# Kernel optimization log

Hardware: AMD Instinct MI355X
Metric: run time of the kernel (lower is better)

Reference implementation:

```python
import jax, jax.numpy as jnp
import numpy as np

DIM = 512
NUM_HEADS = 8
HEAD_DIM = DIM // NUM_HEADS
SCALE = HEAD_DIM ** -0.5


def setup_inputs() -> dict:
    key = jax.random.key(0)
    kx, kqw, kqb, kpw, kpb = jax.random.split(key, 5)
    B, N = 2, 4096
    x = jax.random.normal(kx, (B, N, DIM), dtype=jnp.float32)
    # nn.Linear weights stored as [out, in]; init ~ U(-1/sqrt(in), 1/sqrt(in))
    bound = 1.0 / np.sqrt(DIM)
    qkv_w = jax.random.uniform(kqw, (3 * DIM, DIM), minval=-bound, maxval=bound, dtype=jnp.float32)
    qkv_b = jax.random.uniform(kqb, (3 * DIM,), minval=-bound, maxval=bound, dtype=jnp.float32)
    proj_w = jax.random.uniform(kpw, (DIM, DIM), minval=-bound, maxval=bound, dtype=jnp.float32)
    proj_b = jax.random.uniform(kpb, (DIM,), minval=-bound, maxval=bound, dtype=jnp.float32)
    return {"x": x, "qkv_w": qkv_w, "qkv_b": qkv_b, "proj_w": proj_w, "proj_b": proj_b}


def reference(x, qkv_w, qkv_b, proj_w, proj_b):
    B, N, C = x.shape
    # qkv: [B, N, 3C] -> [3, B, H, N, Dh]
    qkv = x @ qkv_w.T + qkv_b
    qkv = qkv.reshape(B, N, 3, NUM_HEADS, HEAD_DIM).transpose(2, 0, 3, 1, 4)
    q, k, v = qkv[0], qkv[1], qkv[2]
    # scores: [B, H, N, N] (materialized, matching the original math)
    attn = jnp.einsum("bhqd,bhkd->bhqk", q, k) * SCALE
    attn = jax.nn.softmax(attn, axis=-1)
    out = jnp.einsum("bhqk,bhkd->bhqd", attn, v)  # [B, H, N, Dh]
    out = out.transpose(0, 2, 1, 3).reshape(B, N, C)
    return out @ proj_w.T + proj_b
```

## Files before the change

### kernel.cpp

```cpp
#include <hip/hip_runtime.h>
#include <hip/hip_bf16.h>
#include <stdint.h>
#include <stddef.h>

typedef __attribute__((ext_vector_type(8))) short short8;
typedef __attribute__((ext_vector_type(4))) float f32x4;

#define MFMA16(a, b, c) __builtin_amdgcn_mfma_f32_16x16x32_bf16((a), (b), (c), 0, 0, 0)

#define QSCALE 0.1803368801111204f

#if __has_builtin(__builtin_amdgcn_exp2f)
#define EXP2(x) __builtin_amdgcn_exp2f(x)
#else
#define EXP2(x) __builtin_exp2f(x)
#endif

__device__ __forceinline__ float b2f(short x) {
    unsigned u = ((unsigned)(unsigned short)x) << 16;
    float f; __builtin_memcpy(&f, &u, 4); return f;
}
__device__ __forceinline__ short f2b(float f) {
    unsigned u; __builtin_memcpy(&u, &f, 4);
    u = (u + 0x7FFFu + ((u >> 16) & 1u)) >> 16;
    return (short)u;
}
__device__ __forceinline__ unsigned pack2(float a, float b) {
    unsigned ua, ub; __builtin_memcpy(&ua, &a, 4); __builtin_memcpy(&ub, &b, 4);
    return __builtin_amdgcn_perm(ub + 0x8000u, ua + 0x8000u, 0x07060302u);
}
__device__ __forceinline__ short8 load8f(const float* p) {
    const float4 f0 = *(const float4*)p;
    const float4 f1 = *(const float4*)(p + 4);
    short8 r;
    r[0]=f2b(f0.x); r[1]=f2b(f0.y); r[2]=f2b(f0.z); r[3]=f2b(f0.w);
    r[4]=f2b(f1.x); r[5]=f2b(f1.y); r[6]=f2b(f1.z); r[7]=f2b(f1.w);
    return r;
}

__global__ __launch_bounds__(256) void cvt3(
    const float* __restrict__ s0, short* __restrict__ d0, int n0,
    const float* __restrict__ s1, short* __restrict__ d1, int n1,
    const float* __restrict__ s2, short* __restrict__ d2, int n2)
{
    int i = blockIdx.x * 256 + threadIdx.x;
    if (i < n0) { *(short8*)(d0 + (size_t)i * 8) = load8f(s0 + (size_t)i * 8); return; }
    i -= n0;
    if (i < n1) { *(short8*)(d1 + (size_t)i * 8) = load8f(s1 + (size_t)i * 8); return; }
    i -= n1;
    if (i < n2) { *(short8*)(d2 + (size_t)i * 8) = load8f(s2 + (size_t)i * 8); }
}

__global__ __launch_bounds__(256) void qkv_gemm(
    const short* __restrict__ X, const short* __restrict__ W,
    const float* __restrict__ bias,
    short* __restrict__ Qb, short* __restrict__ Kb, short* __restrict__ Vb)
{
    __shared__ short sT[128][132];

    const int tid  = threadIdx.x;
    const int wv   = tid >> 6;
    const int lane = tid & 63;
    const int l15  = lane & 15;
    const int quad = lane >> 4;
    const int m0   = blockIdx.x * 128 + (wv >> 1) * 64;
    const int sec  = blockIdx.y >> 2;
    const int bis  = blockIdx.y & 3;
    const int nbase = sec * 512 + bis * 128;
    const int j0   = (wv & 1) * 64;

    const f32x4 zero = {0.f, 0.f, 0.f, 0.f};
    f32x4 acc[4][4];
#pragma unroll
    for (int i = 0; i < 4; i++)
#pragma unroll
        for (int j = 0; j < 4; j++) acc[i][j] = zero;

    for (int k0 = 0; k0 < 512; k0 += 32) {
        short8 a[4], b[4];
#pragma unroll
        for (int i = 0; i < 4; i++)
            a[i] = *(const short8*)(X + (size_t)(m0 + i * 16 + l15) * 512 + k0 + quad * 8);
#pragma unroll
        for (int j = 0; j < 4; j++)
            b[j] = *(const short8*)(W + (size_t)(nbase + j0 + j * 16 + l15) * 512 + k0 + quad * 8);
#pragma unroll
        for (int i = 0; i < 4; i++)
#pragma unroll
            for (int j = 0; j < 4; j++)
                acc[i][j] = MFMA16(a[i], b[j], acc[i][j]);
    }

    if (sec < 2) {
        const float scale = (sec == 0) ? QSCALE : 1.0f;
        short* dst = (sec == 0) ? Qb : Kb;
#pragma unroll
        for (int j = 0; j < 4; j++) {
            const int jc = bis * 128 + j0 + j * 16 + l15;
            const float bs = bias[sec * 512 + jc];
            const int hl = jc >> 6, d = jc & 63;
#pragma unroll
            for (int i = 0; i < 4; i++) {
#pragma unroll
                for (int r = 0; r < 4; r++) {
                    const int m = m0 + i * 16 + quad * 4 + r;
                    const int bb = m >> 12, seq = m & 4095;
                    dst[((size_t)(bb * 8 + hl) * 4096 + seq) * 64 + d] =
                        f2b((acc[i][j][r] + bs) * scale);
                }
            }
        }
    } else {
#pragma unroll
        for (int j = 0; j < 4; j++) {
            const int jcl = j0 + j * 16 + l15;
            const float bs = bias[nbase + jcl];
#pragma unroll
            for (int i = 0; i < 4; i++) {
                uint2 w;
                w.x = pack2(acc[i][j][0] + bs, acc[i][j][1] + bs);
                w.y = pack2(acc[i][j][2] + bs, acc[i][j][3] + bs);
                *(uint2*)&sT[jcl][(wv >> 1) * 64 + i * 16 + quad * 4] = w;
            }
        }
        __syncthreads();

        const int jcl = tid >> 1, half = tid & 1;
        const int hl = (bis * 128 + jcl) >> 6;
        const int d  = jcl & 63;
        const int bb = (blockIdx.x * 128) >> 12;
        const int seq0 = ((blockIdx.x * 128) & 4095) + half * 64;
        short* dst = Vb + ((size_t)(bb * 8 + hl) * 64 + d) * 4096 + seq0;
#pragma unroll
        for (int u = 0; u < 8; u++)
            *(short8*)(dst + u * 8) = *(const short8*)&sT[jcl][half * 64 + u * 8];
    }
}

__global__ __launch_bounds__(256) void flash_attn(
    const short* __restrict__ Q, const short* __restrict__ K,
    const short* __restrict__ V, short* __restrict__ PO0,
    short* __restrict__ PO1, float* __restrict__ lbuf, int ktiles)
{
    __shared__ short sK[64][72];
    __shared__ short sV[64][72];
    __shared__ short sP[4][16][72];

    const int tid  = threadIdx.x;
    const int wv   = tid >> 6;
    const int lane = tid & 63;
    const int l15  = lane & 15;
    const int quad = lane >> 4;
    const int bh = blockIdx.y;
    const int b = bh >> 3, h = bh & 7;
    const int qw = blockIdx.x * 128 + wv * 32;
    const int ks = blockIdx.z;
    const int key0 = ks * ktiles * 64;

    const short* Qb = Q + (size_t)bh * 4096 * 64;
    const short* Kb = K + (size_t)bh * 4096 * 64;
    const short* Vb = V + (size_t)bh * 64 * 4096;

    const short8 aq00 = *(const short8*)(Qb + (size_t)(qw + l15) * 64 + quad * 8);
    const short8 aq01 = *(const short8*)(Qb + (size_t)(qw + l15) * 64 + 32 + quad * 8);
    const short8 aq10 = *(const short8*)(Qb + (size_t)(qw + 16 + l15) * 64 + quad * 8);
    const short8 aq11 = *(const short8*)(Qb + (size_t)(qw + 16 + l15) * 64 + 32 + quad * 8);

    const f32x4 zero = {0.f, 0.f, 0.f, 0.f};
    f32x4 o0[4], o1[4];
    f32x4 lac0 = zero, lac1 = zero;
#pragma unroll
    for (int r = 0; r < 4; r++) { o0[r] = zero; o1[r] = zero; }
    const short one_bf = (short)0x3F80;
    const short8 ones = {one_bf, one_bf, one_bf, one_bf,
                         one_bf, one_bf, one_bf, one_bf};

    int srow[2], scb[2];
#pragma unroll
    for (int i = 0; i < 2; i++) {
        const int c = tid + i * 256;
        srow[i] = c >> 3; scb[i] = (c & 7) * 8;
    }
    short8 pk[2], pv[2];
#pragma unroll
    for (int i = 0; i < 2; i++) {
        pk[i] = *(const short8*)(Kb + (size_t)(key0 + srow[i]) * 64 + scb[i]);
        pv[i] = *(const short8*)(Vb + (size_t)srow[i] * 4096 + key0 + scb[i]);
    }

    for (int kt = 0; kt < ktiles; ++kt) {
        const int k0 = key0 + kt * 64;
        __syncthreads();
#pragma unroll
        for (int i = 0; i < 2; i++) {
            *(short8*)&sK[srow[i]][scb[i]] = pk[i];
            *(short8*)&sV[srow[i]][scb[i]] = pv[i];
        }
        __syncthreads();

        if (kt + 1 < ktiles) {
            const int k0n = k0 + 64;
#pragma unroll
            for (int i = 0; i < 2; i++) {
                pk[i] = *(const short8*)(Kb + (size_t)(k0n + srow[i]) * 64 + scb[i]);
                pv[i] = *(const short8*)(Vb + (size_t)srow[i] * 4096 + k0n + scb[i]);
            }
        }

        f32x4 ST0[4], ST1[4];
#pragma unroll
        for (int c = 0; c < 4; c++) {
            const short8 bk0 = *(const short8*)&sK[c * 16 + l15][quad * 8];
            const short8 bk1 = *(const short8*)&sK[c * 16 + l15][32 + quad * 8];
            ST0[c] = MFMA16(bk1, aq01, MFMA16(bk0, aq00, zero));
            ST1[c] = MFMA16(bk1, aq11, MFMA16(bk0, aq10, zero));
        }

        short8 bv[4][2];
#pragma unroll
        for (int td = 0; td < 4; td++) {
            bv[td][0] = *(const short8*)&sV[td * 16 + l15][quad * 8];
            bv[td][1] = *(const short8*)&sV[td * 16 + l15][32 + quad * 8];
        }

#pragma unroll
        for (int c = 0; c < 4; c++) {
            uint2 w;
            w.x = pack2(EXP2(ST0[c][0]), EXP2(ST0[c][1]));
            w.y = pack2(EXP2(ST0[c][2]), EXP2(ST0[c][3]));
            *(uint2*)&sP[wv][l15][c * 16 + quad * 4] = w;
        }
        __threadfence_block();
        {
            const short8 bp0 = *(const short8*)&sP[wv][l15][quad * 8];
            const short8 bp1 = *(const short8*)&sP[wv][l15][32 + quad * 8];
            lac0 = MFMA16(ones, bp0, lac0);
            lac0 = MFMA16(ones, bp1, lac0);
#pragma unroll
            for (int td = 0; td < 4; td++) {
                o0[td] = MFMA16(bv[td][0], bp0, o0[td]);
                o0[td] = MFMA16(bv[td][1], bp1, o0[td]);
            }
        }
        __threadfence_block();

#pragma unroll
        for (int c = 0; c < 4; c++) {
            uint2 w;
            w.x = pack2(EXP2(ST1[c][0]), EXP2(ST1[c][1]));
            w.y = pack2(EXP2(ST1[c][2]), EXP2(ST1[c][3]));
            *(uint2*)&sP[wv][l15][c * 16 + quad * 4] = w;
        }
        __threadfence_block();
        {
            const short8 bp0 = *(const short8*)&sP[wv][l15][quad * 8];
            const short8 bp1 = *(const short8*)&sP[wv][l15][32 + quad * 8];
            lac1 = MFMA16(ones, bp0, lac1);
            lac1 = MFMA16(ones, bp1, lac1);
#pragma unroll
            for (int td = 0; td < 4; td++) {
                o1[td] = MFMA16(bv[td][0], bp0, o1[td]);
                o1[td] = MFMA16(bv[td][1], bp1, o1[td]);
            }
        }
    }

    const float l0 = lac0[0];
    const float l1 = lac1[0];
    const float inv0 = 1.f / fmaxf(l0, 1e-30f);
    const float inv1 = 1.f / fmaxf(l1, 1e-30f);

    short* PO = (ks == 0) ? PO0 : PO1;
#pragma unroll
    for (int td = 0; td < 4; td++) {
        uint2 w0, w1;
        w0.x = pack2(o0[td][0] * inv0, o0[td][1] * inv0);
        w0.y = pack2(o0[td][2] * inv0, o0[td][3] * inv0);
        w1.x = pack2(o1[td][0] * inv1, o1[td][1] * inv1);
        w1.y = pack2(o1[td][2] * inv1, o1[td][3] * inv1);
        const int col = h * 64 + td * 16 + quad * 4;
        *(uint2*)(PO + ((size_t)b * 4096 + qw + l15) * 512 + col) = w0;
        *(uint2*)(PO + ((size_t)b * 4096 + qw + 16 + l15) * 512 + col) = w1;
    }
    if (quad == 0) {
        lbuf[((size_t)ks * 16 + bh) * 4096 + qw + l15] = l0;
        lbuf[((size_t)ks * 16 + bh) * 4096 + qw + 16 + l15] = l1;
    }
}

__global__ __launch_bounds__(256) void combine(
    const short* __restrict__ PO0, const short* __restrict__ PO1,
    short* __restrict__ attn, const float* __restrict__ L)
{
    const int i = blockIdx.x * 256 + threadIdx.x;
    const size_t flat = (size_t)i * 8;
    const int col = (int)(flat & 511);
    const int q   = (int)((flat >> 9) & 4095);
    const int b   = (int)(flat >> 21);
    const int bh  = b * 8 + (col >> 6);
    const float l0 = L[(size_t)bh * 4096 + q];
    const float l1 = L[(size_t)65536 + (size_t)bh * 4096 + q];
    const float inv = 1.f / (l0 + l1);
    const float w0 = l0 * inv, w1 = l1 * inv;
    const short8 a = *(const short8*)(PO0 + flat);
    const short8 c = *(const short8*)(PO1 + flat);
    short8 r;
#pragma unroll
    for (int k = 0; k < 8; k += 2) {
        const unsigned p = pack2(w0 * b2f(a[k]) + w1 * b2f(c[k]),
                                 w0 * b2f(a[k + 1]) + w1 * b2f(c[k + 1]));
        r[k]     = (short)(p & 0xFFFF);
        r[k + 1] = (short)(p >> 16);
    }
    *(short8*)(attn + flat) = r;
}

__global__ __launch_bounds__(256) void proj_gemm(
    const short* __restrict__ A, const short* __restrict__ W,
    const float* __restrict__ bias, float* __restrict__ dst)
{
    const int tid  = threadIdx.x;
    const int wv   = tid >> 6;
    const int lane = tid & 63;
    const int l15  = lane & 15;
    const int quad = lane >> 4;
    const int m0 = blockIdx.x * 128 + (wv >> 1) * 64;
    const int n0 = blockIdx.y * 128 + (wv & 1) * 64;

    const f32x4 zero = {0.f, 0.f, 0.f, 0.f};
    f32x4 acc[4][4];
#pragma unroll
    for (int i = 0; i < 4; i++)
#pragma unroll
        for (int j = 0; j < 4; j++) acc[i][j] = zero;

    for (int k0 = 0; k0 < 512; k0 += 32) {
        short8 a[4], b[4];
#pragma unroll
        for (int i = 0; i < 4; i++)
            a[i] = *(const short8*)(A + (size_t)(m0 + i * 16 + l15) * 512 + k0 + quad * 8);
#pragma unroll
        for (int j = 0; j < 4; j++)
            b[j] = *(const short8*)(W + (size_t)(n0 + j * 16 + l15) * 512 + k0 + quad * 8);
#pragma unroll
        for (int i = 0; i < 4; i++)
#pragma unroll
            for (int j = 0; j < 4; j++)
                acc[i][j] = MFMA16(a[i], b[j], acc[i][j]);
    }

#pragma unroll
    for (int j = 0; j < 4; j++) {
        const int n = n0 + j * 16 + l15;
        const float bs = bias[n];
#pragma unroll
        for (int i = 0; i < 4; i++) {
#pragma unroll
            for (int r = 0; r < 4; r++) {
                const int m = m0 + i * 16 + quad * 4 + r;
                dst[(size_t)m * 512 + n] = acc[i][j][r] + bs;
            }
        }
    }
}

extern "C" void kernel_launch(void* const* d_in, const int* in_sizes, int n_in,
                              void* d_out, int out_size, void* d_ws, size_t ws_size,
                              hipStream_t stream)
{
    const float* x      = (const float*)d_in[0];
    const float* qkv_w  = (const float*)d_in[1];
    const float* qkv_b  = (const float*)d_in[2];
    const float* proj_w = (const float*)d_in[3];
    const float* proj_b = (const float*)d_in[4];

    const size_t MB = 1024 * 1024;
    short* xb   = (short*)d_out;
    short* wb   = (short*)d_out + 4 * MB;
    short* PO0  = (short*)d_out;
    short* PO1  = (short*)d_out + 4 * MB;
    float* out  = (float*)d_out;

    short* Qf = (short*)d_ws;
    short* Kf = Qf + (size_t)16 * 4096 * 64;
    short* Vf = Kf + (size_t)16 * 4096 * 64;
    short* attn = Qf;
    float* lbuf = (float*)((char*)d_ws + 24 * MB);
    short* pwb  = (short*)((char*)d_ws + 24 * MB + 512 * 1024);

    cvt3<<<2560, 256, 0, stream>>>(x, xb, 524288, qkv_w, wb, 98304, proj_w, pwb, 32768);
    qkv_gemm<<<dim3(64, 12), 256, 0, stream>>>(xb, wb, qkv_b, Qf, Kf, Vf);
    flash_attn<<<dim3(32, 16, 2), 256, 0, stream>>>(Qf, Kf, Vf, PO0, PO1, lbuf, 32);
    combine<<<2048, 256, 0, stream>>>(PO0, PO1, attn, lbuf);
    proj_gemm<<<dim3(64, 4), 256, 0, stream>>>(attn, pwb, proj_b, out);
}
```

Baseline: 264.4 us.

## Switch flash attention inner loop to 32x32x16 MFMA with scalar row sums

Rewrites the attention inner loop to use 32x32x16 bf16 MFMA tiles instead of 16x16x32. Each wave now handles its 32 query rows in a single pass rather than two 16-row halves. The softmax denominator is accumulated with scalar adds on the exp values instead of extra MFMAs against a ones vector, which removes those MFMAs and halves the sP round trips. The cost is larger 16-wide accumulators that raise register pressure, and a lane-pair shuffle to finish the row sums.

```diff
diff --git a/kernel.cpp b/kernel.cpp
--- a/kernel.cpp
+++ b/kernel.cpp
@@ -5,8 +5,10 @@
 
 typedef __attribute__((ext_vector_type(8))) short short8;
 typedef __attribute__((ext_vector_type(4))) float f32x4;
+typedef __attribute__((ext_vector_type(16))) float f32x16;
 
 #define MFMA16(a, b, c) __builtin_amdgcn_mfma_f32_16x16x32_bf16((a), (b), (c), 0, 0, 0)
+#define MFMA32(a, b, c) __builtin_amdgcn_mfma_f32_32x32x16_bf16((a), (b), (c), 0, 0, 0)
 
 #define QSCALE 0.1803368801111204f
 
@@ -144,13 +146,13 @@
 {
     __shared__ short sK[64][72];
     __shared__ short sV[64][72];
-    __shared__ short sP[4][16][72];
+    __shared__ short sP[4][32][72];
 
     const int tid  = threadIdx.x;
     const int wv   = tid >> 6;
     const int lane = tid & 63;
-    const int l15  = lane & 15;
-    const int quad = lane >> 4;
+    const int l31  = lane & 31;
+    const int half = lane >> 5;
     const int bh = blockIdx.y;
     const int b = bh >> 3, h = bh & 7;
     const int qw = blockIdx.x * 128 + wv * 32;
@@ -161,19 +163,13 @@
     const short* Kb = K + (size_t)bh * 4096 * 64;
     const short* Vb = V + (size_t)bh * 64 * 4096;
 
-    const short8 aq00 = *(const short8*)(Qb + (size_t)(qw + l15) * 64 + quad * 8);
-    const short8 aq01 = *(const short8*)(Qb + (size_t)(qw + l15) * 64 + 32 + quad * 8);
-    const short8 aq10 = *(const short8*)(Qb + (size_t)(qw + 16 + l15) * 64 + quad * 8);
-    const short8 aq11 = *(const short8*)(Qb + (size_t)(qw + 16 + l15) * 64 + 32 + quad * 8);
-
-    const f32x4 zero = {0.f, 0.f, 0.f, 0.f};
-    f32x4 o0[4], o1[4];
-    f32x4 lac0 = zero, lac1 = zero;
-#pragma unroll
-    for (int r = 0; r < 4; r++) { o0[r] = zero; o1[r] = zero; }
-    const short one_bf = (short)0x3F80;
-    const short8 ones = {one_bf, one_bf, one_bf, one_bf,
-                         one_bf, one_bf, one_bf, one_bf};
+    short8 aq[4];
+#pragma unroll
+    for (int s = 0; s < 4; s++)
+        aq[s] = *(const short8*)(Qb + (size_t)(qw + l31) * 64 + s * 16 + half * 8);
+
+    f32x16 o0 = {}, o1 = {};
+    float lsum = 0.f;
 
     int srow[2], scb[2];
 #pragma unroll
@@ -207,85 +203,58 @@
             }
         }
 
-        f32x4 ST0[4], ST1[4];
-#pragma unroll
-        for (int c = 0; c < 4; c++) {
-            const short8 bk0 = *(const short8*)&sK[c * 16 + l15][quad * 8];
-            const short8 bk1 = *(const short8*)&sK[c * 16 + l15][32 + quad * 8];
-            ST0[c] = MFMA16(bk1, aq01, MFMA16(bk0, aq00, zero));
-            ST1[c] = MFMA16(bk1, aq11, MFMA16(bk0, aq10, zero));
-        }
-
-        short8 bv[4][2];
-#pragma unroll
-        for (int td = 0; td < 4; td++) {
-            bv[td][0] = *(const short8*)&sV[td * 16 + l15][quad * 8];
-            bv[td][1] = *(const short8*)&sV[td * 16 + l15][32 + quad * 8];
-        }
-
-#pragma unroll
-        for (int c = 0; c < 4; c++) {
-            uint2 w;
-            w.x = pack2(EXP2(ST0[c][0]), EXP2(ST0[c][1]));
-            w.y = pack2(EXP2(ST0[c][2]), EXP2(ST0[c][3]));
-            *(uint2*)&sP[wv][l15][c * 16 + quad * 4] = w;
+#pragma unroll
+        for (int c = 0; c < 2; c++) {
+            f32x16 ST = {};
+#pragma unroll
+            for (int s = 0; s < 4; s++) {
+                const short8 bk = *(const short8*)&sK[c * 32 + l31][s * 16 + half * 8];
+                ST = MFMA32(bk, aq[s], ST);
+            }
+#pragma unroll
+            for (int q = 0; q < 4; q++) {
+                const float p0 = EXP2(ST[4 * q + 0]), p1 = EXP2(ST[4 * q + 1]);
+                const float p2 = EXP2(ST[4 * q + 2]), p3 = EXP2(ST[4 * q + 3]);
+                lsum += (p0 + p1) + (p2 + p3);
+                uint2 w; w.x = pack2(p0, p1); w.y = pack2(p2, p3);
+                *(uint2*)&sP[wv][l31][c * 32 + q * 8 + half * 4] = w;
+            }
         }
         __threadfence_block();
-        {
-            const short8 bp0 = *(const short8*)&sP[wv][l15][quad * 8];
-            const short8 bp1 = *(const short8*)&sP[wv][l15][32 + quad * 8];
-            lac0 = MFMA16(ones, bp0, lac0);
-            lac0 = MFMA16(ones, bp1, lac0);
-#pragma unroll
-            for (int td = 0; td < 4; td++) {
-                o0[td] = MFMA16(bv[td][0], bp0, o0[td]);
-                o0[td] = MFMA16(bv[td][1], bp1, o0[td]);
-            }
+
+        short8 bp[4];
+#pragma unroll
+        for (int s = 0; s < 4; s++)
+            bp[s] = *(const short8*)&sP[wv][l31][s * 16 + half * 8];
+
+#pragma unroll
+        for (int s = 0; s < 4; s++) {
+            const short8 bv0 = *(const short8*)&sV[l31][s * 16 + half * 8];
+            const short8 bv1 = *(const short8*)&sV[32 + l31][s * 16 + half * 8];
+            o0 = MFMA32(bv0, bp[s], o0);
+            o1 = MFMA32(bv1, bp[s], o1);
         }
         __threadfence_block();
-
-#pragma unroll
-        for (int c = 0; c < 4; c++) {
-            uint2 w;
-            w.x = pack2(EXP2(ST1[c][0]), EXP2(ST1[c][1]));
-            w.y = pack2(EXP2(ST1[c][2]), EXP2(ST1[c][3]));
-            *(uint2*)&sP[wv][l15][c * 16 + quad * 4] = w;
-        }
-        __threadfence_block();
-        {
-            const short8 bp0 = *(const short8*)&sP[wv][l15][quad * 8];
-            const short8 bp1 = *(const short8*)&sP[wv][l15][32 + quad * 8];
-            lac1 = MFMA16(ones, bp0, lac1);
-            lac1 = MFMA16(ones, bp1, lac1);
-#pragma unroll
-            for (int td = 0; td < 4; td++) {
-                o1[td] = MFMA16(bv[td][0], bp0, o1[td]);
-                o1[td] = MFMA16(bv[td][1], bp1, o1[td]);
-            }
-        }
-    }
-
-    const float l0 = lac0[0];
-    const float l1 = lac1[0];
-    const float inv0 = 1.f / fmaxf(l0, 1e-30f);
-    const float inv1 = 1.f / fmaxf(l1, 1e-30f);
+    }
+
+    lsum += __shfl_xor(lsum, 32);
+    const float inv = 1.f / fmaxf(lsum, 1e-30f);
 
     short* PO = (ks == 0) ? PO0 : PO1;
 #pragma unroll
-    for (int td = 0; td < 4; td++) {
+    for (int q = 0; q < 4; q++) {
         uint2 w0, w1;
-        w0.x = pack2(o0[td][0] * inv0, o0[td][1] * inv0);
-        w0.y = pack2(o0[td][2] * inv0, o0[td][3] * inv0);
-        w1.x = pack2(o1[td][0] * inv1, o1[td][1] * inv1);
-        w1.y = pack2(o1[td][2] * inv1, o1[td][3] * inv1);
-        const int col = h * 64 + td * 16 + quad * 4;
-        *(uint2*)(PO + ((size_t)b * 4096 + qw + l15) * 512 + col) = w0;
-        *(uint2*)(PO + ((size_t)b * 4096 + qw + 16 + l15) * 512 + col) = w1;
-    }
-    if (quad == 0) {
-        lbuf[((size_t)ks * 16 + bh) * 4096 + qw + l15] = l0;
-        lbuf[((size_t)ks * 16 + bh) * 4096 + qw + 16 + l15] = l1;
-    }
+        w0.x = pack2(o0[4 * q + 0] * inv, o0[4 * q + 1] * inv);
+        w0.y = pack2(o0[4 * q + 2] * inv, o0[4 * q + 3] * inv);
+        w1.x = pack2(o1[4 * q + 0] * inv, o1[4 * q + 1] * inv);
+        w1.y = pack2(o1[4 * q + 2] * inv, o1[4 * q + 3] * inv);
+        const size_t rowoff = ((size_t)b * 4096 + qw + l31) * 512;
+        const int col = h * 64 + q * 8 + half * 4;
+        *(uint2*)(PO + rowoff + col) = w0;
+        *(uint2*)(PO + rowoff + col + 32) = w1;
+    }
+    if (half == 0)
+        lbuf[((size_t)ks * 16 + bh) * 4096 + qw + l31] = lsum;
 }
 
 __global__ __launch_bounds__(256) void combine(
```

After: 265.0 us. About the same (+0.2%).
